# Performance work log

Measured on AMD Instinct MI355X. Metric: run time of the kernel, lower is better.

The kernel has to match this reference:

```python
import jax, jax.numpy as jnp
import numpy as np

B, DIM, HEADS, HEAD_DIM = 4, 768, 8, 96
THW = (8, 28, 28)
N_TOK = THW[0] * THW[1] * THW[2] + 1  # +1 cls token = 6273
HIDDEN = 4 * DIM
STRIDE = (1, 2, 2)
SCALE = HEAD_DIM ** -0.5


def layernorm(x, w, b, eps=1e-5):
    mu = x.mean(-1, keepdims=True)
    var = ((x - mu) ** 2).mean(-1, keepdims=True)
    return (x - mu) / jnp.sqrt(var + eps) * w + b


def conv_pool(x, w):
    # depthwise 3D conv: x [BN, C, T, H, W], w [C, 1, 3, 3, 3], stride (1,2,2), pad 1
    return jax.lax.conv_general_dilated(
        x, w, window_strides=STRIDE, padding=[(1, 1), (1, 1), (1, 1)],
        dimension_numbers=('NCDHW', 'OIDHW', 'NCDHW'),
        feature_group_count=x.shape[1])


def attn_pool(x, conv_w, norm_w, norm_b):
    # x: [B, h, N, d]; pool spatial tokens (excluding cls), then LayerNorm(head_dim)
    cls, xs = x[:, :, :1], x[:, :, 1:]
    b, h, _, d = xs.shape
    t, hh, ww = THW
    xs = xs.reshape(b * h, t, hh, ww, d).transpose(0, 4, 1, 2, 3)  # [bh, d, t, h, w]
    xs = conv_pool(xs, conv_w)
    l_pooled = xs.shape[2] * xs.shape[3] * xs.shape[4]
    xs = xs.reshape(b, h, d, l_pooled).transpose(0, 1, 3, 2)  # [B, h, L, d]
    xs = jnp.concatenate([cls, xs], axis=2)
    return layernorm(xs, norm_w, norm_b)


def max_pool_skip(x):
    # residual-path MaxPool3d: kernel (1,3,3), stride (1,2,2), pad (0,1,1); cls excluded
    cls, xs = x[:, :1], x[:, 1:]
    b, _, c = xs.shape
    t, hh, ww = THW
    xs = xs.reshape(b, t, hh, ww, c)
    xs = jax.lax.reduce_window(
        xs, -jnp.inf, jax.lax.max,
        (1, 1, 3, 3, 1), (1, 1, 2, 2, 1),
        [(0, 0), (0, 0), (1, 1), (1, 1), (0, 0)])
    xs = xs.reshape(b, -1, c)
    return jnp.concatenate([cls, xs], axis=1)


def setup_inputs() -> dict:
    key = jax.random.key(0)
    ks = jax.random.split(key, 16)
    s = 0.02
    inp = {
        'x': jax.random.normal(ks[0], (B, N_TOK, DIM), jnp.float32),
        'n1_w': jnp.ones((DIM,), jnp.float32), 'n1_b': jnp.zeros((DIM,), jnp.float32),
        'wq': jax.random.normal(ks[1], (DIM, DIM), jnp.float32) * s,
        'bq': jnp.zeros((DIM,), jnp.float32),
        'wk': jax.random.normal(ks[2], (DIM, DIM), jnp.float32) * s,
        'bk': jnp.zeros((DIM,), jnp.float32),
        'wv': jax.random.normal(ks[3], (DIM, DIM), jnp.float32) * s,
        'bv': jnp.zeros((DIM,), jnp.float32),
        'pq_w': jax.random.normal(ks[4], (HEAD_DIM, 1, 3, 3, 3), jnp.float32) * s,
        'pk_w': jax.random.normal(ks[5], (HEAD_DIM, 1, 3, 3, 3), jnp.float32) * s,
        'pv_w': jax.random.normal(ks[6], (HEAD_DIM, 1, 3, 3, 3), jnp.float32) * s,
        'nq_w': jnp.ones((HEAD_DIM,), jnp.float32), 'nq_b': jnp.zeros((HEAD_DIM,), jnp.float32),
        'nk_w': jnp.ones((HEAD_DIM,), jnp.float32), 'nk_b': jnp.zeros((HEAD_DIM,), jnp.float32),
        'nv_w': jnp.ones((HEAD_DIM,), jnp.float32), 'nv_b': jnp.zeros((HEAD_DIM,), jnp.float32),
        'proj_w': jax.random.normal(ks[7], (DIM, DIM), jnp.float32) * s,
        'proj_b': jnp.zeros((DIM,), jnp.float32),
        'n2_w': jnp.ones((DIM,), jnp.float32), 'n2_b': jnp.zeros((DIM,), jnp.float32),
        'fc1_w': jax.random.normal(ks[8], (HIDDEN, DIM), jnp.float32) * s,
        'fc1_b': jnp.zeros((HIDDEN,), jnp.float32),
        'fc2_w': jax.random.normal(ks[9], (DIM, HIDDEN), jnp.float32) * s,
        'fc2_b': jnp.zeros((DIM,), jnp.float32),
    }
    return inp


def reference(x, n1_w, n1_b, wq, bq, wk, bk, wv, bv, pq_w, pk_w, pv_w,
              nq_w, nq_b, nk_w, nk_b, nv_w, nv_b, proj_w, proj_b,
              n2_w, n2_b, fc1_w, fc1_b, fc2_w, fc2_b):
    b, n, _ = x.shape
    xn = layernorm(x, n1_w, n1_b)
    # q/k/v projections -> [B, h, N, d]
    q = (xn @ wq.T + bq).reshape(b, n, HEADS, HEAD_DIM).transpose(0, 2, 1, 3)
    k = (xn @ wk.T + bk).reshape(b, n, HEADS, HEAD_DIM).transpose(0, 2, 1, 3)
    v = (xn @ wv.T + bv).reshape(b, n, HEADS, HEAD_DIM).transpose(0, 2, 1, 3)
    q = attn_pool(q, pq_w, nq_w, nq_b)
    k = attn_pool(k, pk_w, nk_w, nk_b)
    v = attn_pool(v, pv_w, nv_w, nv_b)
    attn = jax.nn.softmax(jnp.einsum('bhqd,bhkd->bhqk', q, k) * SCALE, axis=-1)
    o = jnp.einsum('bhqk,bhkd->bhqd', attn, v)
    nq = o.shape[2]
    o = o.transpose(0, 2, 1, 3).reshape(b, nq, DIM)
    o = o @ proj_w.T + proj_b
    # residual with pooled skip
    x2 = max_pool_skip(x) + o
    xn2 = layernorm(x2, n2_w, n2_b)
    m = jax.nn.gelu(xn2 @ fc1_w.T + fc1_b, approximate=False) @ fc2_w.T + fc2_b
    return x2 + m
```

## Files before the change

### kernel.cpp

```cpp
#include <hip/hip_runtime.h>
#include <math.h>

#define B_ 4
#define NTOK 6273
#define DIMD 768
#define HEADS 8
#define HD 96
#define NPOOL 1569
#define NPAD 1600
#define HID 3072
#define MROWS (B_*NTOK)
#define M2 (B_*NPOOL)
#define SCALE_ 0.10206207261596575f

typedef float f32x4 __attribute__((ext_vector_type(4)));
typedef short s16x8 __attribute__((ext_vector_type(8)));
typedef short s16x4 __attribute__((ext_vector_type(4)));
typedef unsigned u32x3 __attribute__((ext_vector_type(3)));

__device__ __forceinline__ short f2bf(float f){
  unsigned u = __builtin_bit_cast(unsigned, f);
  u = (u + 0x7fffu + ((u >> 16) & 1u)) >> 16;
  return (short)u;
}
__device__ __forceinline__ float bf2f(short s){
  unsigned u = ((unsigned)(unsigned short)s) << 16;
  return __builtin_bit_cast(float, u);
}
__device__ __forceinline__ float bfsel(unsigned u, int hi){
  unsigned r = hi ? (u & 0xffff0000u) : (u << 16);
  return __builtin_bit_cast(float, r);
}
__device__ __forceinline__ unsigned pack2(float lo, float hi){
  return (unsigned)(unsigned short)f2bf(lo) | ((unsigned)(unsigned short)f2bf(hi) << 16);
}

__device__ __forceinline__ void gld16(const void* g, void* l){
  __builtin_amdgcn_global_load_lds((const __attribute__((address_space(1))) unsigned*)g,
                                   (__attribute__((address_space(3))) unsigned*)l, 16, 0, 0);
}

#if defined(__has_builtin)
#if __has_builtin(__builtin_amdgcn_mfma_f32_16x16x16bf16_1k)
#define MFMA16K(a,b,c) __builtin_amdgcn_mfma_f32_16x16x16bf16_1k(a,b,c,0,0,0)
#endif
#endif
#ifndef MFMA16K
__device__ __forceinline__ f32x4 mfma16k_asm(s16x4 a, s16x4 b, f32x4 c){
  asm volatile("v_mfma_f32_16x16x16_bf16 %0, %1, %2, %0\n\ts_nop 7\n\ts_nop 7"
               : "+v"(c) : "v"(a), "v"(b));
  return c;
}
#define MFMA16K(a,b,c) mfma16k_asm(a,b,c)
#endif

template<int NT>
__device__ __forceinline__ float block_sum(float v, float* red){
  int t = threadIdx.x;
  red[t] = v; __syncthreads();
  #pragma unroll
  for (int s = NT/2; s > 0; s >>= 1){
    if (t < s) red[t] += red[t+s];
    __syncthreads();
  }
  float r = red[0];
  __syncthreads();
  return r;
}

__device__ __forceinline__ unsigned xcd_serial(unsigned bid, unsigned nwg){
  unsigned q = nwg >> 3, r8 = nwg & 7;
  unsigned xcd = bid & 7, idx = bid >> 3;
  return (xcd < r8 ? xcd*(q+1) : r8*(q+1) + (xcd-r8)*q) + idx;
}

template<int STR, int STC>
__device__ __forceinline__ void tile_decode(unsigned serial, int& rowT, int& colT){
  const int nStC = (int)gridDim.x / STC;
  int st = (int)serial / (STR*STC);
  int t  = (int)serial - st*(STR*STC);
  int stR = st / nStC, stC = st - stR*nStC;
  int c = t / STR, r = t - c*STR;
  rowT = stR*STR + r;
  colT = stC*STC + c;
}

__global__ void castw(const float* s0,const float* s1,const float* s2,const float* s3,
                      const float* s4,const float* s5,
                      short* d0,short* d1,short* d2,short* d3,short* d4,short* d5){
  const float* s; short* d; int n;
  switch(blockIdx.y){
    case 0: s=s0; d=d0; n=589824; break;
    case 1: s=s1; d=d1; n=589824; break;
    case 2: s=s2; d=d2; n=589824; break;
    case 3: s=s3; d=d3; n=589824; break;
    case 4: s=s4; d=d4; n=2359296; break;
    default: s=s5; d=d5; n=2359296; break;
  }
  for (int i = blockIdx.x*blockDim.x + threadIdx.x; i < n; i += gridDim.x*blockDim.x)
    d[i] = f2bf(s[i]);
}

__global__ __launch_bounds__(256) void packb(const float* b0, const float* b1, const float* b2, float* o){
  int i = blockIdx.x*256 + threadIdx.x;
  if (i < 768) o[i] = b0[i];
  else if (i < 1536) o[i] = b1[i-768];
  else if (i < 2304) o[i] = b2[i-1536];
}

__global__ __launch_bounds__(256) void ln768(const float* __restrict__ x, const float* __restrict__ w,
                      const float* __restrict__ b, short* __restrict__ out){
  int row = blockIdx.x*4 + (threadIdx.x >> 6);
  int lane = threadIdx.x & 63;
  const float* xr = x + (size_t)row*DIMD + lane*12;
  f32x4 v0 = *(const f32x4*)(xr);
  f32x4 v1 = *(const f32x4*)(xr + 4);
  f32x4 v2 = *(const f32x4*)(xr + 8);
  float v[12] = { v0[0],v0[1],v0[2],v0[3], v1[0],v1[1],v1[2],v1[3], v2[0],v2[1],v2[2],v2[3] };
  float s = 0.f;
  #pragma unroll
  for (int j=0;j<12;j++) s += v[j];
  #pragma unroll
  for (int m=1; m<64; m<<=1) s += __shfl_xor(s, m);
  float mu = s * (1.f/768.f);
  float sq = 0.f;
  #pragma unroll
  for (int j=0;j<12;j++){ float d = v[j]-mu; sq += d*d; }
  #pragma unroll
  for (int m=1; m<64; m<<=1) sq += __shfl_xor(sq, m);
  float rstd = rsqrtf(sq*(1.f/768.f) + 1e-5f);
  int c0 = lane*12;
  float o[12];
  #pragma unroll
  for (int j=0;j<12;j++) o[j] = (v[j]-mu)*rstd*w[c0+j] + b[c0+j];
  unsigned* po = (unsigned*)(out + (size_t)row*DIMD + c0);
  #pragma unroll
  for (int k=0;k<6;k++) po[k] = pack2(o[2*k], o[2*k+1]);
}

template<int GELU, int OUTBF16, int RESID, int STR, int STC>
__global__ __launch_bounds__(256) void gemm_bt(const short* __restrict__ A, const short* __restrict__ Bw,
                        const float* __restrict__ bias, const float* __restrict__ resid,
                        float* __restrict__ Cf, short* __restrict__ Cb,
                        int M, int N, int K){
  __shared__ short lds[3][8192];
  int tid = threadIdx.x;
  int lane = tid & 63, wv = tid >> 6;
  int wr = wv >> 1, wc = wv & 1;
  int l15 = lane & 15, g = lane >> 4;

  unsigned nwg = gridDim.x * gridDim.y;
  unsigned bid = blockIdx.y * gridDim.x + blockIdx.x;
  unsigned serial = xcd_serial(bid, nwg);
  int rowT, colT;
  tile_decode<STR,STC>(serial, rowT, colT);
  int rowBase = rowT * 128;
  int colBase = colT * 128;

  f32x4 acc[4][4] = {};
  int srow = (tid & 15) | ((tid >> 6) << 4);
  int scol = ((tid >> 4) & 3) * 8;
  int ldsoff = tid * 8;

  int ar0 = rowBase + srow;      if (ar0 >= M) ar0 = M-1;
  int ar1 = rowBase + srow + 64; if (ar1 >= M) ar1 = M-1;
  int br0 = colBase + srow;
  const short* pa0 = A  + (size_t)ar0*K + scol;
  const short* pa1 = A  + (size_t)ar1*K + scol;
  const short* pb0 = Bw + (size_t)br0*K + scol;
  const short* pb1 = Bw + (size_t)(br0+64)*K + scol;

  auto stage = [&](int s, int kt){
    gld16(pa0 + kt, &lds[s][ldsoff]);
    gld16(pa1 + kt, &lds[s][ldsoff + 2048]);
    gld16(pb0 + kt, &lds[s][4096 + ldsoff]);
    gld16(pb1 + kt, &lds[s][4096 + ldsoff + 2048]);
  };

  int nk = K >> 5;
  stage(0, 0);
  if (nk > 1) stage(1, 32);
  for (int kt = 0; kt < nk; kt++){
    int cur = kt % 3;
    if (kt + 2 < nk){
      stage((kt+2)%3, (kt+2)*32);
      asm volatile("s_waitcnt vmcnt(8)" ::: "memory");
    } else if (kt + 1 < nk){
      asm volatile("s_waitcnt vmcnt(4)" ::: "memory");
    } else {
      asm volatile("s_waitcnt vmcnt(0)" ::: "memory");
    }
    __builtin_amdgcn_s_barrier();
    const short* la = lds[cur];
    const short* lb = lds[cur] + 4096;
    s16x8 af[4], bfr[4];
    #pragma unroll
    for (int m=0;m<4;m++) af[m]  = *(const s16x8*)(la + (wr*4 + m)*512 + g*128 + l15*8);
    #pragma unroll
    for (int n=0;n<4;n++) bfr[n] = *(const s16x8*)(lb + (wc*4 + n)*512 + g*128 + l15*8);
    #pragma unroll
    for (int m=0;m<4;m++)
      #pragma unroll
      for (int n=0;n<4;n++)
        acc[m][n] = __builtin_amdgcn_mfma_f32_16x16x32_bf16(af[m], bfr[n], acc[m][n], 0,0,0);
    __builtin_amdgcn_s_barrier();
  }

  if (OUTBF16){
    short* ldsC = &lds[0][0];
    #pragma unroll
    for (int n=0;n<4;n++){
      int colL = wc*64 + n*16 + l15;
      float bv = bias[colBase + colL];
      #pragma unroll
      for (int m=0;m<4;m++){
        #pragma unroll
        for (int r=0;r<4;r++){
          int rowL = wr*64 + m*16 + g*4 + r;
          float v = acc[m][n][r] + bv;
          if (GELU) v = 0.5f*v*(1.f + erff(v*0.70710678118654752f));
          int ch = colL >> 3, in8 = colL & 7;
          int chs = ch ^ (((rowL >> 2) & 3) << 2);
          ldsC[rowL*128 + chs*8 + in8] = f2bf(v);
        }
      }
    }
    __syncthreads();
    int ch = tid & 15, rg = tid >> 4;
    #pragma unroll
    for (int i=0;i<8;i++){
      int rowL = rg + i*16;
      int chs = ch ^ (((rowL >> 2) & 3) << 2);
      s16x8 v = *(const s16x8*)(ldsC + rowL*128 + chs*8);
      int rr = rowBase + rowL;
      if (rr < M) *(s16x8*)(Cb + (size_t)rr*N + colBase + ch*8) = v;
    }
  } else {
    #pragma unroll
    for (int m=0;m<4;m++){
      int row = rowBase + wr*64 + m*16 + g*4;
      #pragma unroll
      for (int n=0;n<4;n++){
        int col = colBase + wc*64 + n*16 + l15;
        float bv = bias[col];
        #pragma unroll
        for (int r=0;r<4;r++){
          int rr = row + r;
          if (rr < M){
            float v = acc[m][n][r] + bv;
            if (GELU) v = 0.5f*v*(1.f + erff(v*0.70710678118654752f));
            if (RESID) v += resid[(size_t)rr*N + col];
            Cf[(size_t)rr*N + col] = v;
          }
        }
      }
    }
  }
}

__global__ __launch_bounds__(256, 2) void pool_conv3(
    const short* __restrict__ raw,
    const float* __restrict__ cwq, const float* __restrict__ cwk, const float* __restrict__ cwv,
    const float* __restrict__ nqw, const float* __restrict__ nqb,
    const float* __restrict__ nkw, const float* __restrict__ nkb,
    const float* __restrict__ nvw, const float* __restrict__ nvb,
    short* __restrict__ qo, short* __restrict__ ko, short* __restrict__ vo){
  unsigned nwg = gridDim.x * gridDim.y * gridDim.z;
  unsigned lin = (blockIdx.z*gridDim.y + blockIdx.y)*gridDim.x + blockIdx.x;
  unsigned serial = xcd_serial(lin, nwg);
  int ho = (int)(serial % 14);
  unsigned rest = serial / 14;
  int bh = (int)(rest & 31);
  int z  = (int)(rest >> 5);
  int t = threadIdx.x;
  int g = t >> 4;
  if (g >= 14) return;
  int s = t & 15, d = s*6;
  const float* cw = (z==0) ? cwq : (z==1) ? cwk : cwv;
  const float* nw = (z==0) ? nqw : (z==1) ? nkw : nvw;
  const float* nb = (z==0) ? nqb : (z==1) ? nkb : nvb;
  const short* base = raw + (size_t)(bh>>3)*NTOK*2304 + z*768 + (bh&7)*96 + d;
  float acc[8][6] = {};
  #pragma unroll
  for (int dh=0; dh<3; dh++){
    int ih = 2*ho - 1 + dh;
    if (ih < 0 || ih >= 28) continue;
    #pragma unroll
    for (int dw=0; dw<3; dw++){
      int iw = 2*g - 1 + dw;
      if (iw < 0 || iw >= 28) continue;
      float w[3][6];
      #pragma unroll
      for (int dt=0; dt<3; dt++)
        #pragma unroll
        for (int j=0;j<6;j++)
          w[dt][j] = cw[(d+j)*27 + dt*9 + dh*3 + dw];
      #pragma unroll
      for (int it=0; it<8; it++){
        u32x3 u = *(const u32x3*)(base + (size_t)(1 + (it*28+ih)*28 + iw)*2304);
        float in[6] = { bfsel(u[0],0), bfsel(u[0],1), bfsel(u[1],0),
                        bfsel(u[1],1), bfsel(u[2],0), bfsel(u[2],1) };
        #pragma unroll
        for (int dt=0; dt<3; dt++){
          int to = it + 1 - dt;
          if (to < 0 || to > 7) continue;
          #pragma unroll
          for (int j=0;j<6;j++) acc[to][j] = fmaf(in[j], w[dt][j], acc[to][j]);
        }
      }
    }
  }
  float nwv[6], nbv[6];
  #pragma unroll
  for (int j=0;j<6;j++){ nwv[j] = nw[d+j]; nbv[j] = nb[d+j]; }
  #pragma unroll
  for (int to=0; to<8; to++){
    float sm = acc[to][0]+acc[to][1]+acc[to][2]+acc[to][3]+acc[to][4]+acc[to][5];
    #pragma unroll
    for (int m=1; m<16; m<<=1) sm += __shfl_xor(sm, m);
    float mu = sm*(1.f/96.f);
    float vr = 0.f;
    #pragma unroll
    for (int j=0;j<6;j++){ float dd = acc[to][j]-mu; vr += dd*dd; }
    #pragma unroll
    for (int m=1; m<16; m<<=1) vr += __shfl_xor(vr, m);
    float rstd = rsqrtf(vr*(1.f/96.f) + 1e-5f);
    int tok = 1 + to*196 + ho*14 + g;
    if (z == 0){
      short o[6];
      #pragma unroll
      for (int j=0;j<6;j++) o[j] = f2bf((acc[to][j]-mu)*rstd*nwv[j] + nbv[j]);
      unsigned* q32 = (unsigned*)(qo + ((size_t)bh*NPAD + tok)*96 + d);
      #pragma unroll
      for (int w2=0; w2<3; w2++)
        q32[w2] = (unsigned)(unsigned short)o[2*w2] | ((unsigned)(unsigned short)o[2*w2+1] << 16);
    } else if (z == 1){
      size_t kb = (size_t)bh*NPAD*96 + (size_t)(tok>>4)*1536 + (tok&15)*8;
      #pragma unroll
      for (int j=0;j<6;j++){
        int dj = d + j;
        ko[kb + (dj>>5)*512 + ((dj>>3)&3)*128 + (dj&7)] = f2bf((acc[to][j]-mu)*rstd*nwv[j] + nbv[j]);
      }
    } else {
      size_t vb = (size_t)bh*NPAD*96 + (size_t)(tok>>6)*6144 + ((tok>>4)&3)*256 + ((tok>>2)&3)*64 + (tok&3);
      #pragma unroll
      for (int j=0;j<6;j++){
        int dj = d + j;
        vo[vb + (dj>>4)*1024 + (dj&15)*4] = f2bf((acc[to][j]-mu)*rstd*nwv[j] + nbv[j]);
      }
    }
  }
}

__global__ __launch_bounds__(128) void cls3(
    const short* __restrict__ raw,
    const float* __restrict__ nqw, const float* __restrict__ nqb,
    const float* __restrict__ nkw, const float* __restrict__ nkb,
    const float* __restrict__ nvw, const float* __restrict__ nvb,
    short* __restrict__ qo, short* __restrict__ ko, short* __restrict__ vo){
  int b = blockIdx.x, t = threadIdx.x;
  int h = t >> 4, s = t & 15, d = s*6;
  int bh = b*8 + h;
  const float* nws[3] = { nqw, nkw, nvw };
  const float* nbs[3] = { nqb, nkb, nvb };
  #pragma unroll
  for (int ten=0; ten<3; ten++){
    const short* row = raw + (size_t)b*NTOK*2304 + ten*768 + h*96 + d;
    u32x3 u = *(const u32x3*)(row);
    float a[6] = { bfsel(u[0],0), bfsel(u[0],1), bfsel(u[1],0), bfsel(u[1],1), bfsel(u[2],0), bfsel(u[2],1) };
    float sm = a[0]+a[1]+a[2]+a[3]+a[4]+a[5];
    #pragma unroll
    for (int m=1; m<16; m<<=1) sm += __shfl_xor(sm, m);
    float mu = sm*(1.f/96.f);
    float vr2 = 0.f;
    #pragma unroll
    for (int j=0;j<6;j++){ float dd = a[j]-mu; vr2 += dd*dd; }
    #pragma unroll
    for (int m=1; m<16; m<<=1) vr2 += __shfl_xor(vr2, m);
    float rstd = rsqrtf(vr2*(1.f/96.f) + 1e-5f);
    #pragma unroll
    for (int j=0;j<6;j++){
      int dj = d + j;
      short o = f2bf((a[j]-mu)*rstd*nws[ten][dj] + nbs[ten][dj]);
      if (ten == 0)      qo[((size_t)bh*NPAD)*96 + dj] = o;
      else if (ten == 1) ko[(size_t)bh*NPAD*96 + (dj>>5)*512 + ((dj>>3)&3)*128 + (dj&7)] = o;
      else               vo[(size_t)bh*NPAD*96 + (dj>>4)*1024 + (dj&15)*4] = o;
    }
  }
}

__global__ __launch_bounds__(96) void padfill(short* __restrict__ qo, short* __restrict__ ko, short* __restrict__ vo){
  int tok = NPOOL + blockIdx.x;
  int bh = blockIdx.y;
  int d = threadIdx.x;
  qo[((size_t)bh*NPAD + tok)*96 + d] = 0;
  size_t kb = (size_t)bh*NPAD*96 + (size_t)(tok>>4)*1536 + (tok&15)*8;
  ko[kb + (d>>5)*512 + ((d>>3)&3)*128 + (d&7)] = 0;
  size_t vb = (size_t)bh*NPAD*96 + (size_t)(tok>>6)*6144 + ((tok>>4)&3)*256 + ((tok>>2)&3)*64 + (tok&3);
  vo[vb + (d>>4)*1024 + (d&15)*4] = 0;
}

__global__ __launch_bounds__(512) void attn_k(const short* __restrict__ qp, const short* __restrict__ kp,
                       const short* __restrict__ vp, short* __restrict__ oattn){
  const float M0 = 6.0f;
  __shared__ short lkv[2][12288];
  unsigned nwg = gridDim.x * gridDim.y;
  unsigned bid0 = blockIdx.y * gridDim.x + blockIdx.x;
  unsigned serial = xcd_serial(bid0, nwg);
  int bh = (int)(serial / 13);
  int qblk = (int)(serial - (unsigned)bh*13);
  int b = bh >> 3, h = bh & 7;
  int tid = threadIdx.x;
  int lane = tid & 63, wv = tid >> 6;
  int l15 = lane & 15, g = lane >> 4;
  int qi = qblk*128 + wv*16 + l15;
  int qi_ld = qi < NPAD ? qi : NPAD-1;
  const short* qbase = qp + (size_t)bh*NPAD*HD;
  const short* kbase = kp + (size_t)bh*NPAD*HD;
  const short* vbase = vp + (size_t)bh*NPAD*HD;
  s16x8 qf[3];
  #pragma unroll
  for (int f=0; f<3; f++)
    qf[f] = *(const s16x8*)(qbase + (size_t)qi_ld*HD + f*32 + g*8);

  auto stage = [&](int bsel, int t){
    #pragma unroll
    for (int i=0;i<3;i++){
      int off = i*4096 + tid*8;
      const short* src = (off < 6144) ? (kbase + t*6144 + off) : (vbase + t*6144 + off - 6144);
      gld16(src, &lkv[bsel][off]);
    }
  };

  f32x4 accO[6] = {};
  float tsum = 0.f;

  stage(0, 0);
  asm volatile("s_waitcnt vmcnt(0)" ::: "memory");
  __builtin_amdgcn_s_barrier();

  for (int kt = 0; kt < 25; kt++){
    int cur = kt & 1;
    if (kt < 24){
      stage(cur^1, kt+1);
      asm volatile("s_waitcnt vmcnt(3)" ::: "memory");
    } else {
      asm volatile("s_waitcnt vmcnt(0)" ::: "memory");
    }
    __builtin_amdgcn_s_barrier();

    const short* lkc = &lkv[cur][0];
    const short* lvc = &lkv[cur][6144];
    f32x4 sacc[4];
    #pragma unroll
    for (int sub=0; sub<4; sub++){
      sacc[sub] = (f32x4){0.f,0.f,0.f,0.f};
      #pragma unroll
      for (int f=0; f<3; f++){
        s16x8 kf = *(const s16x8*)(lkc + sub*1536 + f*512 + lane*8);
        sacc[sub] = __builtin_amdgcn_mfma_f32_16x16x32_bf16(kf, qf[f], sacc[sub], 0,0,0);
      }
    }
    s16x4 pf[4];
    if (kt < 24){
      #pragma unroll
      for (int sub=0; sub<4; sub++){
        #pragma unroll
        for (int r=0; r<4; r++){
          float p = __expf(sacc[sub][r]*SCALE_ - M0);
          tsum += p;
          pf[sub][r] = f2bf(p);
        }
      }
    } else {
      #pragma unroll
      for (int sub=0; sub<4; sub++){
        #pragma unroll
        for (int r=0; r<4; r++){
          int ki = kt*64 + sub*16 + g*4 + r;
          float p = (ki < NPOOL) ? __expf(sacc[sub][r]*SCALE_ - M0) : 0.f;
          tsum += p;
          pf[sub][r] = f2bf(p);
        }
      }
    }
    #pragma unroll
    for (int dt=0; dt<6; dt++){
      #pragma unroll
      for (int sub=0; sub<4; sub++){
        s16x4 vf = *(const s16x4*)(lvc + dt*1024 + sub*256 + lane*4);
        accO[dt] = MFMA16K(vf, pf[sub], accO[dt]);
      }
    }
    __builtin_amdgcn_s_barrier();
  }

  tsum += __shfl_xor(tsum, 16);
  tsum += __shfl_xor(tsum, 32);
  if (qi < NPOOL){
    float inv = 1.f / tsum;
    #pragma unroll
    for (int dt=0; dt<6; dt++){
      #pragma unroll
      for (int r=0; r<4; r++){
        int dd = dt*16 + g*4 + r;
        oattn[((size_t)b*NPOOL + qi)*DIMD + h*96 + dd] = f2bf(accO[dt][r] * inv);
      }
    }
  }
}

__global__ __launch_bounds__(256) void skip_ln2(const float* __restrict__ x, const float* __restrict__ oproj,
                         const float* __restrict__ w, const float* __restrict__ bb,
                         float* __restrict__ x2, short* __restrict__ xn2){
  unsigned nwg = gridDim.x * gridDim.y;
  unsigned bid = blockIdx.y * gridDim.x + blockIdx.x;
  unsigned serial = xcd_serial(bid, nwg);
  int b = (int)(serial / NPOOL);
  int tok = (int)(serial - (unsigned)b*NPOOL);
  int t = threadIdx.x;
  __shared__ float red[256];
  float v[3];
  int ot = tok - 1;
  int to = ot/196, rem = ot%196, ho = rem/14, wo = rem%14;
  #pragma unroll
  for (int i=0;i<3;i++){
    int c = t + i*256;
    float mv;
    if (tok == 0){
      mv = x[(size_t)b*NTOK*DIMD + c];
    } else {
      mv = -INFINITY;
      #pragma unroll
      for (int dh=0; dh<3; dh++){
        int ih = 2*ho - 1 + dh; if (ih < 0 || ih >= 28) continue;
        #pragma unroll
        for (int dw=0; dw<3; dw++){
          int iw = 2*wo - 1 + dw; if (iw < 0 || iw >= 28) continue;
          int n = 1 + (to*28 + ih)*28 + iw;
          mv = fmaxf(mv, x[((size_t)b*NTOK + n)*DIMD + c]);
        }
      }
    }
    float val = mv + oproj[((size_t)b*NPOOL + tok)*DIMD + c];
    x2[((size_t)b*NPOOL + tok)*DIMD + c] = val;
    v[i] = val;
  }
  float s = v[0]+v[1]+v[2];
  s = block_sum<256>(s, red);
  float mu = s * (1.f/768.f);
  float sq = 0.f;
  #pragma unroll
  for (int i=0;i<3;i++){ float d = v[i]-mu; sq += d*d; }
  sq = block_sum<256>(sq, red);
  float rstd = rsqrtf(sq*(1.f/768.f) + 1e-5f);
  #pragma unroll
  for (int i=0;i<3;i++){
    int c = t + i*256;
    xn2[((size_t)b*NPOOL + tok)*DIMD + c] = f2bf((v[i]-mu)*rstd*w[c] + bb[c]);
  }
}

extern "C" void kernel_launch(void* const* d_in, const int* in_sizes, int n_in,
                              void* d_out, int out_size, void* d_ws, size_t ws_size,
                              hipStream_t stream){
  (void)in_sizes; (void)n_in; (void)out_size; (void)ws_size;
  const float* x      = (const float*)d_in[0];
  const float* n1_w   = (const float*)d_in[1];
  const float* n1_b   = (const float*)d_in[2];
  const float* wq     = (const float*)d_in[3];
  const float* bq     = (const float*)d_in[4];
  const float* wk     = (const float*)d_in[5];
  const float* bk     = (const float*)d_in[6];
  const float* wv     = (const float*)d_in[7];
  const float* bv     = (const float*)d_in[8];
  const float* pq_w   = (const float*)d_in[9];
  const float* pk_w   = (const float*)d_in[10];
  const float* pv_w   = (const float*)d_in[11];
  const float* nq_w   = (const float*)d_in[12];
  const float* nq_b   = (const float*)d_in[13];
  const float* nk_w   = (const float*)d_in[14];
  const float* nk_b   = (const float*)d_in[15];
  const float* nv_w   = (const float*)d_in[16];
  const float* nv_b   = (const float*)d_in[17];
  const float* proj_w = (const float*)d_in[18];
  const float* proj_b = (const float*)d_in[19];
  const float* n2_w   = (const float*)d_in[20];
  const float* n2_b   = (const float*)d_in[21];
  const float* fc1_w  = (const float*)d_in[22];
  const float* fc1_b  = (const float*)d_in[23];
  const float* fc2_w  = (const float*)d_in[24];
  const float* fc2_b  = (const float*)d_in[25];
  float* out = (float*)d_out;

  char* ws = (char*)d_ws;
  size_t off = 0;
  auto take = [&](size_t bytes)->char*{
    char* p = ws + off; off = (off + bytes + 255) & ~(size_t)255; return p;
  };
  short* xn  = (short*)take(38541312);
  short* wqb = (short*)take(1179648);
  short* wkb = (short*)take(1179648);
  short* wvb = (short*)take(1179648);
  short* wpb = (short*)take(1179648);
  short* w1b = (short*)take(4718592);
  short* w2b = (short*)take(4718592);
  float* bcat= (float*)take(9216);
  char*  big = take(115623936);
  short* qkv  = (short*)(big);
  short* oattn= (short*)(big);
  float* oproj= (float*)(big + 9639936);
  float* x2   = (float*)(big + 28919808);
  short* xn2  = (short*)(big + 48199680);
  short* h1   = (short*)(big + 57839616);
  short* qp   = (short*)take(9830400);
  short* kp   = (short*)take(9830400);
  short* vT   = (short*)take(9830400);

  castw<<<dim3(2304,6), 256, 0, stream>>>(wq,wk,wv,proj_w,fc1_w,fc2_w, wqb,wkb,wvb,wpb,w1b,w2b);
  packb<<<9, 256, 0, stream>>>(bq, bk, bv, bcat);
  ln768<<<6273, 256, 0, stream>>>(x, n1_w, n1_b, xn);

  gemm_bt<0,1,0,1,18><<<dim3(18,197), 256, 0, stream>>>(xn, wqb, bcat, nullptr, nullptr, qkv, MROWS, 2304, 768);

  pool_conv3<<<dim3(32,14,3), 256, 0, stream>>>(qkv, pq_w, pk_w, pv_w,
                                                nq_w, nq_b, nk_w, nk_b, nv_w, nv_b, qp, kp, vT);
  cls3<<<dim3(B_), 128, 0, stream>>>(qkv, nq_w, nq_b, nk_w, nk_b, nv_w, nv_b, qp, kp, vT);
  padfill<<<dim3(31,32), 96, 0, stream>>>(qp, kp, vT);

  attn_k<<<dim3(13,32), 512, 0, stream>>>(qp, kp, vT, oattn);

  gemm_bt<0,0,0,10,6><<<dim3(6,50), 256, 0, stream>>>(oattn, wpb, proj_b, nullptr, oproj, nullptr, M2, 768, 768);

  skip_ln2<<<dim3(NPOOL,B_), 256, 0, stream>>>(x, oproj, n2_w, n2_b, x2, xn2);

  gemm_bt<1,1,0,10,8><<<dim3(24,50), 256, 0, stream>>>(xn2, w1b, fc1_b, nullptr, nullptr, h1, M2, HID, 768);
  gemm_bt<0,0,1,2,3><<<dim3(6,50), 256, 0, stream>>>(h1, w2b, fc2_b, x2, out, nullptr, M2, 768, HID);
}
```

Measured before the change: 628.0 us.

## Add 256x256-tile 8-wave GEMM with 4-stage LDS pipeline for QKV projection

Replaces the QKV projection GEMM with a new kernel using 512 threads and 256x256 output tiles. It runs a 4-slot LDS ring with three stages of loads in flight and fine-grained vmcnt waits, and stages the epilogue through swizzled LDS so bf16 stores are coalesced. The larger tile raises arithmetic intensity and cuts redundant global loads of A and B. The cost is 128KB of LDS per block and high register use, which lowers occupancy and can leave a tail imbalance across the 891 blocks.

Measured after the change: 614.6 us. 1.02x faster.

```diff
diff --git a/kernel.cpp b/kernel.cpp
--- a/kernel.cpp
+++ b/kernel.cpp
@@ -136,6 +136,103 @@
   unsigned* po = (unsigned*)(out + (size_t)row*DIMD + c0);
   #pragma unroll
   for (int k=0;k<6;k++) po[k] = pack2(o[2*k], o[2*k+1]);
+}
+
+__global__ __launch_bounds__(512) void gemm8(const short* __restrict__ A, const short* __restrict__ Bw,
+                        const float* __restrict__ bias, short* __restrict__ Cb,
+                        int M, int N, int K){
+  __shared__ short lds[4][16384];
+  int tid = threadIdx.x;
+  int w = tid >> 6, lane = tid & 63;
+  int l15 = lane & 15, g = (lane >> 4) & 3;
+  int wr = w >> 2, wc = w & 3;
+
+  unsigned nwg = gridDim.x * gridDim.y;
+  unsigned bid = blockIdx.y * gridDim.x + blockIdx.x;
+  unsigned serial = bid;
+  if (nwg >= 512) serial = xcd_serial(bid, nwg);
+  int rowBase = (int)(serial / gridDim.x) * 256;
+  int colBase = (int)(serial % gridDim.x) * 256;
+
+  const short* pa[2]; const short* pb[2];
+  #pragma unroll
+  for (int j=0;j<2;j++){
+    int mr = rowBase + (w + j*8)*16 + l15; if (mr >= M) mr = M-1;
+    int nr = colBase + (w + j*8)*16 + l15;
+    pa[j] = A  + (size_t)mr*K + g*8;
+    pb[j] = Bw + (size_t)nr*K + g*8;
+  }
+  int sd = tid*8;
+
+  auto stage = [&](int slot, int p){
+    int koff = p*32;
+    short* base = &lds[slot][0];
+    #pragma unroll
+    for (int j=0;j<2;j++){
+      gld16(pa[j] + koff, base + sd + j*4096);
+      gld16(pb[j] + koff, base + 8192 + sd + j*4096);
+    }
+  };
+
+  f32x4 acc[8][4] = {};
+  int np = K >> 5;
+  stage(0, 0);
+  if (np > 1) stage(1, 1);
+  if (np > 2) stage(2, 2);
+  for (int p = 0; p < np; p++){
+    if (p <= np-3)
+      asm volatile("s_waitcnt vmcnt(8)" ::: "memory");
+    else if (p == np-2)
+      asm volatile("s_waitcnt vmcnt(4)" ::: "memory");
+    else
+      asm volatile("s_waitcnt vmcnt(0)" ::: "memory");
+    __builtin_amdgcn_s_barrier();
+    if (p + 3 < np) stage((p+3)&3, p+3);
+    const short* lA = &lds[p&3][0];
+    const short* lB = lA + 8192;
+    s16x8 bfr[4];
+    #pragma unroll
+    for (int nf=0; nf<4; nf++)
+      bfr[nf] = *(const s16x8*)(lB + (wc*4+nf)*512 + lane*8);
+    __builtin_amdgcn_s_setprio(1);
+    #pragma unroll
+    for (int mf=0; mf<8; mf++){
+      s16x8 af = *(const s16x8*)(lA + (wr*8+mf)*512 + lane*8);
+      #pragma unroll
+      for (int nf=0; nf<4; nf++)
+        acc[mf][nf] = __builtin_amdgcn_mfma_f32_16x16x32_bf16(af, bfr[nf], acc[mf][nf], 0,0,0);
+    }
+    __builtin_amdgcn_s_setprio(0);
+  }
+
+  __syncthreads();
+  short* ldsC = &lds[0][0];
+  #pragma unroll
+  for (int mf=0; mf<8; mf++){
+    int rowL0 = wr*128 + mf*16 + g*4;
+    #pragma unroll
+    for (int nf=0; nf<4; nf++){
+      int colL = wc*64 + nf*16 + l15;
+      float bv = bias[colBase + colL];
+      int ch = colL >> 3, in8 = colL & 7;
+      #pragma unroll
+      for (int r=0;r<4;r++){
+        int rL = rowL0 + r;
+        int chs = ch ^ ((rL >> 2) & 7);
+        ldsC[rL*256 + chs*8 + in8] = f2bf(acc[mf][nf][r] + bv);
+      }
+    }
+  }
+  __syncthreads();
+  int ch2 = tid & 31, rg = tid >> 5;
+  #pragma unroll
+  for (int i=0;i<16;i++){
+    int rowL = rg + i*16;
+    int chs = ch2 ^ ((rowL >> 2) & 7);
+    s16x8 v = *(const s16x8*)(ldsC + rowL*256 + chs*8);
+    int rr = rowBase + rowL;
+    if (rr < M) *(s16x8*)(Cb + (size_t)rr*N + colBase + ch2*8) = v;
+  }
 }
 
 template<int GELU, int OUTBF16, int RESID, int STR, int STC>
@@ -621,7 +718,7 @@
   packb<<<9, 256, 0, stream>>>(bq, bk, bv, bcat);
   ln768<<<6273, 256, 0, stream>>>(x, n1_w, n1_b, xn);
 
-  gemm_bt<0,1,0,1,18><<<dim3(18,197), 256, 0, stream>>>(xn, wqb, bcat, nullptr, nullptr, qkv, MROWS, 2304, 768);
+  gemm8<<<dim3(9,99), 512, 0, stream>>>(xn, wqb, bcat, qkv, MROWS, 2304, 768);
 
   pool_conv3<<<dim3(32,14,3), 256, 0, stream>>>(qkv, pq_w, pk_w, pv_w,
                                                 nq_w, nq_b, nk_w, nk_b, nv_w, nv_b, qp, kp, vT);
```
